# Kernel optimization log

Hardware: AMD Instinct MI355X
Metric: run time of the kernel (lower is better)

The kernel has to match this reference:

```python
import jax, jax.numpy as jnp
import numpy as np

D_MODEL, D_HIDDEN, N_EXPERTS, TOP_K = 1024, 2048, 8, 2


def setup_inputs() -> dict:
    key = jax.random.key(0)
    ks = jax.random.split(key, 8)
    s_in = 1.0 / np.sqrt(D_MODEL)
    s_hid = 1.0 / np.sqrt(D_HIDDEN)
    return {
        "x": jax.random.normal(ks[0], (1, 2048, D_MODEL), dtype=jnp.float32),
        # stacked expert weights, stored (in, out) so y = x @ W + b
        "W1": jax.random.normal(ks[1], (N_EXPERTS, D_MODEL, D_HIDDEN), dtype=jnp.float32) * s_in,
        "b1": jnp.zeros((N_EXPERTS, D_HIDDEN), dtype=jnp.float32),
        "W2": jax.random.normal(ks[2], (N_EXPERTS, D_MODEL, D_HIDDEN), dtype=jnp.float32) * s_in,
        "b2": jnp.zeros((N_EXPERTS, D_HIDDEN), dtype=jnp.float32),
        "Wo": jax.random.normal(ks[3], (N_EXPERTS, D_HIDDEN, D_MODEL), dtype=jnp.float32) * s_hid,
        "bo": jnp.zeros((N_EXPERTS, D_MODEL), dtype=jnp.float32),
        "Wr": jax.random.normal(ks[4], (D_MODEL, N_EXPERTS), dtype=jnp.float32) * s_in,
        "br": jnp.zeros((N_EXPERTS,), dtype=jnp.float32),
    }


def reference(x, W1, b1, W2, b2, Wo, bo, Wr, br):
    B, S, D = x.shape
    T = B * S
    xf = x.reshape(T, D)

    # router
    logits = xf @ Wr + br                      # [T, E]
    probs = jax.nn.softmax(logits, axis=-1)
    topk_probs, topk_idx = jax.lax.top_k(probs, TOP_K)  # [T, K]

    # combine weights: c[t, e] = sum_k topk_probs[t, k] * 1[topk_idx[t, k] == e]
    c = jnp.zeros((T, N_EXPERTS), dtype=xf.dtype)
    c = c.at[jnp.arange(T)[:, None], topk_idx].add(topk_probs)  # [T, E]

    # per-expert SwiGLU FFN applied densely, then masked-combined (same math
    # as the original gather/scatter loop since c[t,e]=0 for unrouted experts)
    h = jnp.einsum('td,edh->eth', xf, W1) + b1[:, None, :]   # [E, T, H]
    g = jnp.einsum('td,edh->eth', xf, W2) + b2[:, None, :]
    y = jnp.einsum('eth,ehd->etd', h * jax.nn.silu(g), Wo) + bo[:, None, :]
    out = jnp.einsum('etd,te->td', y, c).reshape(B, S, D)

    probs_mean = probs.mean(axis=0)
    lb_loss = (probs_mean * probs_mean).sum() * N_EXPERTS
    return out, lb_loss
```

## Files before the change

### kernel.cpp

```cpp
#include <hip/hip_runtime.h>
#include <hip/hip_bf16.h>

#define T_TOK 2048
#define DM 1024
#define DH 2048
#define NE 8

using bf16x8 = __attribute__((ext_vector_type(8))) short;
using f32x4  = __attribute__((ext_vector_type(4))) float;

__device__ __forceinline__ unsigned short f2bf(float f) {
  union { float f; unsigned u; } v; v.f = f;
  unsigned r = v.u + 0x7FFFu + ((v.u >> 16) & 1u);
  return (unsigned short)(r >> 16);
}
__device__ __forceinline__ unsigned pk2(float a, float b) {
  return (unsigned)f2bf(a) | ((unsigned)f2bf(b) << 16);
}

__global__ void k_init(int* __restrict__ cnt) {
  if (threadIdx.x < NE) cnt[threadIdx.x] = 0;
}

__global__ __launch_bounds__(64) void k_router(
    const float* __restrict__ x, const float* __restrict__ Wr, const float* __restrict__ br,
    int* __restrict__ cnt, int* __restrict__ idx, float* __restrict__ wgt,
    int* __restrict__ t2r, float* __restrict__ probs, unsigned short* __restrict__ xb)
{
  const int t = blockIdx.x, l = threadIdx.x;
  float xv[16];
#pragma unroll
  for (int i = 0; i < 16; ++i) xv[i] = x[t*DM + l + 64*i];
#pragma unroll
  for (int i = 0; i < 16; ++i) xb[t*DM + l + 64*i] = f2bf(xv[i]);

  float acc[8] = {0.f,0.f,0.f,0.f,0.f,0.f,0.f,0.f};
#pragma unroll
  for (int i = 0; i < 16; ++i) {
    const float4* wp = (const float4*)&Wr[(size_t)(l + 64*i)*NE];
    float4 wa = wp[0], wb = wp[1];
    acc[0] += xv[i]*wa.x; acc[1] += xv[i]*wa.y; acc[2] += xv[i]*wa.z; acc[3] += xv[i]*wa.w;
    acc[4] += xv[i]*wb.x; acc[5] += xv[i]*wb.y; acc[6] += xv[i]*wb.z; acc[7] += xv[i]*wb.w;
  }
#pragma unroll
  for (int e = 0; e < 8; ++e) {
#pragma unroll
    for (int off = 32; off; off >>= 1) acc[e] += __shfl_xor(acc[e], off, 64);
    acc[e] += br[e];
  }
  float mx = acc[0];
#pragma unroll
  for (int e = 1; e < 8; ++e) mx = fmaxf(mx, acc[e]);
  float p[8], s = 0.f;
#pragma unroll
  for (int e = 0; e < 8; ++e) { p[e] = expf(acc[e] - mx); s += p[e]; }
  float inv = 1.f / s;
#pragma unroll
  for (int e = 0; e < 8; ++e) p[e] *= inv;

  int e0 = 0; float p0 = p[0];
#pragma unroll
  for (int e = 1; e < 8; ++e) if (p[e] > p0) { p0 = p[e]; e0 = e; }
  int e1 = -1; float p1 = -1.f;
#pragma unroll
  for (int e = 0; e < 8; ++e) { if (e == e0) continue; if (p[e] > p1) { p1 = p[e]; e1 = e; } }

  if (l == 0) {
#pragma unroll
    for (int e = 0; e < 8; ++e) probs[t*NE + e] = p[e];
    int pos0 = atomicAdd(&cnt[e0], 1);
    idx[e0*T_TOK + pos0] = t; wgt[e0*T_TOK + pos0] = p0;
    t2r[t*2 + 0] = e0*T_TOK + pos0;
    int pos1 = atomicAdd(&cnt[e1], 1);
    idx[e1*T_TOK + pos1] = t; wgt[e1*T_TOK + pos1] = p1;
    t2r[t*2 + 1] = e1*T_TOK + pos1;
  }
}

__global__ __launch_bounds__(256) void k_finalize(
    const int* __restrict__ cnt, int* __restrict__ rb,
    const float* __restrict__ probs, float* __restrict__ out)
{
  __shared__ float red[8][256];
  const int tid = threadIdx.x;
  float s[8] = {0.f,0.f,0.f,0.f,0.f,0.f,0.f,0.f};
  for (int t = tid; t < T_TOK; t += 256) {
#pragma unroll
    for (int e = 0; e < 8; ++e) s[e] += probs[t*NE + e];
  }
#pragma unroll
  for (int e = 0; e < 8; ++e) red[e][tid] = s[e];
  __syncthreads();
  for (int w = 128; w > 0; w >>= 1) {
    if (tid < w) {
#pragma unroll
      for (int e = 0; e < 8; ++e) red[e][tid] += red[e][tid + w];
    }
    __syncthreads();
  }
  if (tid == 0) {
    float lb = 0.f;
#pragma unroll
    for (int e = 0; e < 8; ++e) {
      float mean = red[e][0] * (1.f / T_TOK);
      lb += mean * mean;
    }
    out[2097152] = lb * NE;
    int r = 0;
#pragma unroll
    for (int e = 0; e < 8; ++e) { rb[e] = r; r += cnt[e]; }
  }
}

#define TM1 128
#define TN1 64
#define BKK 64

__global__ __launch_bounds__(256) void k_ffn1(
    const unsigned short* __restrict__ xb,
    const float* __restrict__ W1, const float* __restrict__ b1,
    const float* __restrict__ W2, const float* __restrict__ b2,
    const int* __restrict__ cnt, const int* __restrict__ rbp,
    const int* __restrict__ idx, unsigned short* __restrict__ act)
{
  const int e = blockIdx.z, mt = blockIdx.y, nt = blockIdx.x;
  const int Me = cnt[e];
  const int m0 = mt * TM1;
  if (m0 >= Me) return;
  const int n0 = nt * TN1;

  __shared__ __align__(16) unsigned short As[TM1*BKK];
  __shared__ __align__(16) unsigned short Bh[TN1*BKK];
  __shared__ __align__(16) unsigned short Bg[TN1*BKK];
  __shared__ int toks[TM1];

  const int tid = threadIdx.x;
  if (tid < TM1) toks[tid] = idx[e*T_TOK + min(m0 + tid, Me - 1)];
  __syncthreads();

  const int lane = tid & 63;
  const int wave = tid >> 6;
  const int wm = wave >> 1, wn = wave & 1;
  const int row16 = lane & 15, kg = lane >> 4;

  f32x4 ah[4][2], ag[4][2];
#pragma unroll
  for (int i = 0; i < 4; ++i)
#pragma unroll
    for (int j = 0; j < 2; ++j) { ah[i][j] = 0.f; ag[i][j] = 0.f; }

  for (int k0 = 0; k0 < DM; k0 += BKK) {
#pragma unroll
    for (int it = 0; it < 4; ++it) {
      int task = tid + it*256;
      int r = task >> 3, sl = task & 7;
      uint4 v = *(const uint4*)&xb[(size_t)toks[r]*DM + k0 + sl*8];
      *(uint4*)&As[r*BKK + ((sl ^ (r & 7)) * 8)] = v;
    }
#pragma unroll
    for (int it = 0; it < 2; ++it) {
      int task = tid + it*256;
      int n = task & 63, kq = (task >> 6) & 7;
      size_t gb = ((size_t)e*DM + (size_t)(k0 + kq*8)) * DH + (n0 + n);
      {
        float f0=W1[gb], f1=W1[gb+DH], f2=W1[gb+2*DH], f3=W1[gb+3*DH];
        float f4=W1[gb+4*DH], f5=W1[gb+5*DH], f6=W1[gb+6*DH], f7=W1[gb+7*DH];
        uint4 v; v.x=pk2(f0,f1); v.y=pk2(f2,f3); v.z=pk2(f4,f5); v.w=pk2(f6,f7);
        *(uint4*)&Bh[n*BKK + ((kq ^ (n & 7)) * 8)] = v;
      }
      {
        float f0=W2[gb], f1=W2[gb+DH], f2=W2[gb+2*DH], f3=W2[gb+3*DH];
        float f4=W2[gb+4*DH], f5=W2[gb+5*DH], f6=W2[gb+6*DH], f7=W2[gb+7*DH];
        uint4 v; v.x=pk2(f0,f1); v.y=pk2(f2,f3); v.z=pk2(f4,f5); v.w=pk2(f6,f7);
        *(uint4*)&Bg[n*BKK + ((kq ^ (n & 7)) * 8)] = v;
      }
    }
    __syncthreads();
#pragma unroll
    for (int ks = 0; ks < 2; ++ks) {
      const int kslot = ks*4 + kg;
      bf16x8 a[4], vbh[2], vbg[2];
#pragma unroll
      for (int mi = 0; mi < 4; ++mi) {
        int m = wm*64 + mi*16 + row16;
        a[mi] = *(const bf16x8*)&As[m*BKK + ((kslot ^ (m & 7)) * 8)];
      }
#pragma unroll
      for (int ni = 0; ni < 2; ++ni) {
        int n = wn*32 + ni*16 + row16;
        int off = n*BKK + ((kslot ^ (n & 7)) * 8);
        vbh[ni] = *(const bf16x8*)&Bh[off];
        vbg[ni] = *(const bf16x8*)&Bg[off];
      }
#pragma unroll
      for (int mi = 0; mi < 4; ++mi)
#pragma unroll
        for (int ni = 0; ni < 2; ++ni) {
          ah[mi][ni] = __builtin_amdgcn_mfma_f32_16x16x32_bf16(a[mi], vbh[ni], ah[mi][ni], 0, 0, 0);
          ag[mi][ni] = __builtin_amdgcn_mfma_f32_16x16x32_bf16(a[mi], vbg[ni], ag[mi][ni], 0, 0, 0);
        }
    }
    __syncthreads();
  }

  const int rb = rbp[e];
#pragma unroll
  for (int mi = 0; mi < 4; ++mi) {
#pragma unroll
    for (int i = 0; i < 4; ++i) {
      int rloc = wm*64 + mi*16 + (lane >> 4)*4 + i;
      int m = m0 + rloc;
      if (m < Me) {
#pragma unroll
        for (int ni = 0; ni < 2; ++ni) {
          int col = n0 + wn*32 + ni*16 + row16;
          float h = ah[mi][ni][i] + b1[e*DH + col];
          float g = ag[mi][ni][i] + b2[e*DH + col];
          float sg = g / (1.f + __expf(-g));
          act[(size_t)(rb + m)*DH + col] = f2bf(h * sg);
        }
      }
    }
  }
}

__global__ __launch_bounds__(256) void k_ffn2(
    const unsigned short* __restrict__ act,
    const float* __restrict__ Wo, const float* __restrict__ bo,
    const int* __restrict__ cnt, const int* __restrict__ rbp,
    float* __restrict__ ys)
{
  const int e = blockIdx.z, mt = blockIdx.y, nt = blockIdx.x;
  const int Me = cnt[e];
  const int m0 = mt * TM1;
  if (m0 >= Me) return;
  const int n0 = nt * TN1;
  const int rb = rbp[e];

  __shared__ __align__(16) unsigned short As[TM1*BKK];
  __shared__ __align__(16) unsigned short Bs[TN1*BKK];

  const int tid = threadIdx.x;
  const int lane = tid & 63;
  const int wave = tid >> 6;
  const int wm = wave >> 1, wn = wave & 1;
  const int row16 = lane & 15, kg = lane >> 4;

  f32x4 acc[4][2];
#pragma unroll
  for (int i = 0; i < 4; ++i)
#pragma unroll
    for (int j = 0; j < 2; ++j) acc[i][j] = 0.f;

  for (int k0 = 0; k0 < DH; k0 += BKK) {
#pragma unroll
    for (int it = 0; it < 4; ++it) {
      int task = tid + it*256;
      int r = task >> 3, sl = task & 7;
      int grow = rb + min(m0 + r, Me - 1);
      uint4 v = *(const uint4*)&act[(size_t)grow*DH + k0 + sl*8];
      *(uint4*)&As[r*BKK + ((sl ^ (r & 7)) * 8)] = v;
    }
#pragma unroll
    for (int it = 0; it < 2; ++it) {
      int task = tid + it*256;
      int n = task & 63, kq = (task >> 6) & 7;
      size_t gb = ((size_t)e*DH + (size_t)(k0 + kq*8)) * DM + (n0 + n);
      float f0=Wo[gb], f1=Wo[gb+DM], f2=Wo[gb+2*DM], f3=Wo[gb+3*DM];
      float f4=Wo[gb+4*DM], f5=Wo[gb+5*DM], f6=Wo[gb+6*DM], f7=Wo[gb+7*DM];
      uint4 v; v.x=pk2(f0,f1); v.y=pk2(f2,f3); v.z=pk2(f4,f5); v.w=pk2(f6,f7);
      *(uint4*)&Bs[n*BKK + ((kq ^ (n & 7)) * 8)] = v;
    }
    __syncthreads();
#pragma unroll
    for (int ks = 0; ks < 2; ++ks) {
      const int kslot = ks*4 + kg;
      bf16x8 a[4], b[2];
#pragma unroll
      for (int mi = 0; mi < 4; ++mi) {
        int m = wm*64 + mi*16 + row16;
        a[mi] = *(const bf16x8*)&As[m*BKK + ((kslot ^ (m & 7)) * 8)];
      }
#pragma unroll
      for (int ni = 0; ni < 2; ++ni) {
        int n = wn*32 + ni*16 + row16;
        b[ni] = *(const bf16x8*)&Bs[n*BKK + ((kslot ^ (n & 7)) * 8)];
      }
#pragma unroll
      for (int mi = 0; mi < 4; ++mi)
#pragma unroll
        for (int ni = 0; ni < 2; ++ni)
          acc[mi][ni] = __builtin_amdgcn_mfma_f32_16x16x32_bf16(a[mi], b[ni], acc[mi][ni], 0, 0, 0);
    }
    __syncthreads();
  }

#pragma unroll
  for (int mi = 0; mi < 4; ++mi) {
#pragma unroll
    for (int i = 0; i < 4; ++i) {
      int rloc = wm*64 + mi*16 + (lane >> 4)*4 + i;
      int m = m0 + rloc;
      if (m < Me) {
#pragma unroll
        for (int ni = 0; ni < 2; ++ni) {
          int col = n0 + wn*32 + ni*16 + row16;
          ys[(size_t)(rb + m)*DM + col] = acc[mi][ni][i] + bo[e*DM + col];
        }
      }
    }
  }
}

__global__ __launch_bounds__(256) void k_combine(
    const float* __restrict__ ys, const int* __restrict__ t2r,
    const int* __restrict__ rbp, const float* __restrict__ wgt,
    float* __restrict__ out)
{
  const int t = blockIdx.x, tid = threadIdx.x;
  const int c0 = t2r[t*2 + 0], c1 = t2r[t*2 + 1];
  const float w0 = wgt[c0], w1 = wgt[c1];
  const int r0 = rbp[c0 >> 11] + (c0 & 2047);
  const int r1 = rbp[c1 >> 11] + (c1 & 2047);
  const float4* p0 = (const float4*)&ys[(size_t)r0*DM];
  const float4* p1 = (const float4*)&ys[(size_t)r1*DM];
  float4* po = (float4*)&out[(size_t)t*DM];
  float4 a = p0[tid], b = p1[tid];
  float4 r;
  r.x = w0*a.x + w1*b.x; r.y = w0*a.y + w1*b.y;
  r.z = w0*a.z + w1*b.z; r.w = w0*a.w + w1*b.w;
  po[tid] = r;
}

extern "C" void kernel_launch(void* const* d_in, const int* in_sizes, int n_in,
                              void* d_out, int out_size, void* d_ws, size_t ws_size,
                              hipStream_t stream)
{
  const float* x  = (const float*)d_in[0];
  const float* W1 = (const float*)d_in[1];
  const float* b1 = (const float*)d_in[2];
  const float* W2 = (const float*)d_in[3];
  const float* b2 = (const float*)d_in[4];
  const float* Wo = (const float*)d_in[5];
  const float* bo = (const float*)d_in[6];
  const float* Wr = (const float*)d_in[7];
  const float* br = (const float*)d_in[8];
  float* out = (float*)d_out;

  char* ws = (char*)d_ws;
  int*   cnt   = (int*)(ws + 0);
  int*   rb    = (int*)(ws + 256);
  int*   t2r   = (int*)(ws + 512);
  int*   idx   = (int*)(ws + 32*1024);
  float* wgt   = (float*)(ws + 96*1024);
  float* probs = (float*)(ws + 160*1024);
  unsigned short* xb  = (unsigned short*)(ws + 256*1024);
  unsigned short* act = (unsigned short*)(ws + 5ull*1024*1024);
  float* ysb = (float*)(ws + 21ull*1024*1024);

  k_init<<<1, 64, 0, stream>>>(cnt);
  k_router<<<T_TOK, 64, 0, stream>>>(x, Wr, br, cnt, idx, wgt, t2r, probs, xb);
  k_finalize<<<1, 256, 0, stream>>>(cnt, rb, probs, out);
  k_ffn1<<<dim3(DH/TN1, T_TOK/TM1, NE), 256, 0, stream>>>(xb, W1, b1, W2, b2, cnt, rb, idx, act);
  k_ffn2<<<dim3(DM/TN1, T_TOK/TM1, NE), 256, 0, stream>>>(act, Wo, bo, cnt, rb, ysb);
  k_combine<<<T_TOK, 256, 0, stream>>>(ysb, t2r, rb, wgt, out);
}
```

Measured before the change: 224.1 us.

## Pre-transpose expert weights to bf16 and stream GEMM tiles via global_load_lds

Adds a transpose-and-convert kernel that rewrites W1, W2 and Wo each call into bf16, K-contiguous copies held in workspace. New FFN GEMM kernels load A and B tiles straight into XOR-swizzled LDS with 16-byte global_load_lds, instead of loading fp32 weights and converting them inside the GEMM. The aim is to halve weight bytes per tile reload and drop in-loop conversion and register staging. The price is a full extra pass that reads the fp32 weights and writes the bf16 copies on every call. The new path runs only when the workspace holds at least 136 MB, otherwise the old kernels run.

```diff
diff --git a/kernel.cpp b/kernel.cpp
--- a/kernel.cpp
+++ b/kernel.cpp
@@ -17,6 +17,11 @@
 __device__ __forceinline__ unsigned pk2(float a, float b) {
   return (unsigned)f2bf(a) | ((unsigned)f2bf(b) << 16);
 }
+
+#define GLOAD16(gsrc, ldst)                                                        \
+  __builtin_amdgcn_global_load_lds(                                                \
+      (const __attribute__((address_space(1))) unsigned int*)(gsrc),               \
+      (__attribute__((address_space(3))) unsigned int*)(ldst), 16, 0, 0)
 
 __global__ void k_init(int* __restrict__ cnt) {
   if (threadIdx.x < NE) cnt[threadIdx.x] = 0;
@@ -112,9 +117,223 @@
   }
 }
 
+__global__ __launch_bounds__(256) void k_convT(
+    const float* __restrict__ in, unsigned short* __restrict__ outT, int R, int C)
+{
+  const int e = blockIdx.z;
+  const int r0 = blockIdx.y * 64, c0 = blockIdx.x * 64;
+  __shared__ float t[64][65];
+  const int tid = threadIdx.x;
+  const int lr = tid >> 4, lc = (tid & 15) * 4;
+#pragma unroll
+  for (int i = 0; i < 4; ++i) {
+    float4 v = *(const float4*)&in[((size_t)e*R + r0 + lr + i*16)*C + c0 + lc];
+    t[lr + i*16][lc+0] = v.x; t[lr + i*16][lc+1] = v.y;
+    t[lr + i*16][lc+2] = v.z; t[lr + i*16][lc+3] = v.w;
+  }
+  __syncthreads();
+  const int oc = tid >> 3;
+  const int od = (tid & 7) * 8;
+#pragma unroll
+  for (int i = 0; i < 2; ++i) {
+    int c = oc + i*32;
+    uint4 v;
+    v.x = pk2(t[od+0][c], t[od+1][c]);
+    v.y = pk2(t[od+2][c], t[od+3][c]);
+    v.z = pk2(t[od+4][c], t[od+5][c]);
+    v.w = pk2(t[od+6][c], t[od+7][c]);
+    *(uint4*)&outT[((size_t)e*C + c0 + c)*R + r0 + od] = v;
+  }
+}
+
 #define TM1 128
 #define TN1 64
 #define BKK 64
+
+
+__global__ __launch_bounds__(256) void k_ffn1b(
+    const unsigned short* __restrict__ xb,
+    const unsigned short* __restrict__ W1T, const float* __restrict__ b1,
+    const unsigned short* __restrict__ W2T, const float* __restrict__ b2,
+    const int* __restrict__ cnt, const int* __restrict__ rbp,
+    const int* __restrict__ idx, unsigned short* __restrict__ act)
+{
+  const int e = blockIdx.z, mt = blockIdx.y, nt = blockIdx.x;
+  const int Me = cnt[e];
+  const int m0 = mt * TM1;
+  if (m0 >= Me) return;
+  const int n0 = nt * TN1;
+
+  __shared__ __align__(16) unsigned short As[TM1*BKK];
+  __shared__ __align__(16) unsigned short Bh[TN1*BKK];
+  __shared__ __align__(16) unsigned short Bg[TN1*BKK];
+  __shared__ int toks[TM1];
+
+  const int tid = threadIdx.x;
+  if (tid < TM1) toks[tid] = idx[e*T_TOK + min(m0 + tid, Me - 1)];
+  __syncthreads();
+
+  const int lane = tid & 63;
+  const int wave = tid >> 6;
+  const int wm = wave >> 1, wn = wave & 1;
+  const int row16 = lane & 15, kg = lane >> 4;
+  const int sl = lane & 7;
+  const int lr = lane >> 3;
+
+  f32x4 ah[4][2], ag[4][2];
+#pragma unroll
+  for (int i = 0; i < 4; ++i)
+#pragma unroll
+    for (int j = 0; j < 2; ++j) { ah[i][j] = 0.f; ag[i][j] = 0.f; }
+
+  for (int k0 = 0; k0 < DM; k0 += BKK) {
+#pragma unroll
+    for (int i = 0; i < 4; ++i) {
+      int r = (wave*4 + i)*8 + lr;
+      const unsigned short* src = &xb[(size_t)toks[r]*DM + k0 + ((sl ^ (r & 7)) * 8)];
+      GLOAD16(src, &As[(wave*4 + i)*512]);
+    }
+#pragma unroll
+    for (int j = 0; j < 2; ++j) {
+      int r = (wave*2 + j)*8 + lr;
+      size_t gb = ((size_t)e*DH + n0 + r)*DM + k0 + ((sl ^ (r & 7)) * 8);
+      GLOAD16(&W1T[gb], &Bh[(wave*2 + j)*512]);
+      GLOAD16(&W2T[gb], &Bg[(wave*2 + j)*512]);
+    }
+    __syncthreads();
+#pragma unroll
+    for (int ks = 0; ks < 2; ++ks) {
+      const int kslot = ks*4 + kg;
+      bf16x8 a[4], vbh[2], vbg[2];
+#pragma unroll
+      for (int mi = 0; mi < 4; ++mi) {
+        int m = wm*64 + mi*16 + row16;
+        a[mi] = *(const bf16x8*)&As[m*BKK + ((kslot ^ (m & 7)) * 8)];
+      }
+#pragma unroll
+      for (int ni = 0; ni < 2; ++ni) {
+        int n = wn*32 + ni*16 + row16;
+        int off = n*BKK + ((kslot ^ (n & 7)) * 8);
+        vbh[ni] = *(const bf16x8*)&Bh[off];
+        vbg[ni] = *(const bf16x8*)&Bg[off];
+      }
+#pragma unroll
+      for (int mi = 0; mi < 4; ++mi)
+#pragma unroll
+        for (int ni = 0; ni < 2; ++ni) {
+          ah[mi][ni] = __builtin_amdgcn_mfma_f32_16x16x32_bf16(a[mi], vbh[ni], ah[mi][ni], 0, 0, 0);
+          ag[mi][ni] = __builtin_amdgcn_mfma_f32_16x16x32_bf16(a[mi], vbg[ni], ag[mi][ni], 0, 0, 0);
+        }
+    }
+    __syncthreads();
+  }
+
+  const int rb = rbp[e];
+#pragma unroll
+  for (int mi = 0; mi < 4; ++mi) {
+#pragma unroll
+    for (int i = 0; i < 4; ++i) {
+      int rloc = wm*64 + mi*16 + (lane >> 4)*4 + i;
+      int m = m0 + rloc;
+      if (m < Me) {
+#pragma unroll
+        for (int ni = 0; ni < 2; ++ni) {
+          int col = n0 + wn*32 + ni*16 + row16;
+          float h = ah[mi][ni][i] + b1[e*DH + col];
+          float g = ag[mi][ni][i] + b2[e*DH + col];
+          float sg = g / (1.f + __expf(-g));
+          act[(size_t)(rb + m)*DH + col] = f2bf(h * sg);
+        }
+      }
+    }
+  }
+}
+
+__global__ __launch_bounds__(256) void k_ffn2b(
+    const unsigned short* __restrict__ act,
+    const unsigned short* __restrict__ WoT, const float* __restrict__ bo,
+    const int* __restrict__ cnt, const int* __restrict__ rbp,
+    float* __restrict__ ys)
+{
+  const int e = blockIdx.z, mt = blockIdx.y, nt = blockIdx.x;
+  const int Me = cnt[e];
+  const int m0 = mt * TM1;
+  if (m0 >= Me) return;
+  const int n0 = nt * TN1;
+  const int rb = rbp[e];
+
+  __shared__ __align__(16) unsigned short As[TM1*BKK];
+  __shared__ __align__(16) unsigned short Bs[TN1*BKK];
+
+  const int tid = threadIdx.x;
+  const int lane = tid & 63;
+  const int wave = tid >> 6;
+  const int wm = wave >> 1, wn = wave & 1;
+  const int row16 = lane & 15, kg = lane >> 4;
+  const int sl = lane & 7;
+  const int lr = lane >> 3;
+
+  f32x4 acc[4][2];
+#pragma unroll
+  for (int i = 0; i < 4; ++i)
+#pragma unroll
+    for (int j = 0; j < 2; ++j) acc[i][j] = 0.f;
+
+  for (int k0 = 0; k0 < DH; k0 += BKK) {
+#pragma unroll
+    for (int i = 0; i < 4; ++i) {
+      int r = (wave*4 + i)*8 + lr;
+      int grow = rb + min(m0 + r, Me - 1);
+      const unsigned short* src = &act[(size_t)grow*DH + k0 + ((sl ^ (r & 7)) * 8)];
+      GLOAD16(src, &As[(wave*4 + i)*512]);
+    }
+#pragma unroll
+    for (int j = 0; j < 2; ++j) {
+      int r = (wave*2 + j)*8 + lr;
+      size_t gb = ((size_t)e*DM + n0 + r)*DH + k0 + ((sl ^ (r & 7)) * 8);
+      GLOAD16(&WoT[gb], &Bs[(wave*2 + j)*512]);
+    }
+    __syncthreads();
+#pragma unroll
+    for (int ks = 0; ks < 2; ++ks) {
+      const int kslot = ks*4 + kg;
+      bf16x8 a[4], b[2];
+#pragma unroll
+      for (int mi = 0; mi < 4; ++mi) {
+        int m = wm*64 + mi*16 + row16;
+        a[mi] = *(const bf16x8*)&As[m*BKK + ((kslot ^ (m & 7)) * 8)];
+      }
+#pragma unroll
+      for (int ni = 0; ni < 2; ++ni) {
+        int n = wn*32 + ni*16 + row16;
+        b[ni] = *(const bf16x8*)&Bs[n*BKK + ((kslot ^ (n & 7)) * 8)];
+      }
+#pragma unroll
+      for (int mi = 0; mi < 4; ++mi)
+#pragma unroll
+        for (int ni = 0; ni < 2; ++ni)
+          acc[mi][ni] = __builtin_amdgcn_mfma_f32_16x16x32_bf16(a[mi], b[ni], acc[mi][ni], 0, 0, 0);
+    }
+    __syncthreads();
+  }
+
+#pragma unroll
+  for (int mi = 0; mi < 4; ++mi) {
+#pragma unroll
+    for (int i = 0; i < 4; ++i) {
+      int rloc = wm*64 + mi*16 + (lane >> 4)*4 + i;
+      int m = m0 + rloc;
+      if (m < Me) {
+#pragma unroll
+        for (int ni = 0; ni < 2; ++ni) {
+          int col = n0 + wn*32 + ni*16 + row16;
+          ys[(size_t)(rb + m)*DM + col] = acc[mi][ni][i] + bo[e*DM + col];
+        }
+      }
+    }
+  }
+}
+
 
 __global__ __launch_bounds__(256) void k_ffn1(
     const unsigned short* __restrict__ xb,
@@ -357,11 +576,24 @@
   unsigned short* xb  = (unsigned short*)(ws + 256*1024);
   unsigned short* act = (unsigned short*)(ws + 5ull*1024*1024);
   float* ysb = (float*)(ws + 21ull*1024*1024);
+  unsigned short* W1T = (unsigned short*)(ws + 40ull*1024*1024);
+  unsigned short* W2T = (unsigned short*)(ws + 72ull*1024*1024);
+  unsigned short* WoT = (unsigned short*)(ws + 104ull*1024*1024);
+  const bool fast = ws_size >= 136ull*1024*1024;
 
   k_init<<<1, 64, 0, stream>>>(cnt);
   k_router<<<T_TOK, 64, 0, stream>>>(x, Wr, br, cnt, idx, wgt, t2r, probs, xb);
   k_finalize<<<1, 256, 0, stream>>>(cnt, rb, probs, out);
-  k_ffn1<<<dim3(DH/TN1, T_TOK/TM1, NE), 256, 0, stream>>>(xb, W1, b1, W2, b2, cnt, rb, idx, act);
-  k_ffn2<<<dim3(DM/TN1, T_TOK/TM1, NE), 256, 0, stream>>>(act, Wo, bo, cnt, rb, ysb);
+
+  if (fast) {
+    k_convT<<<dim3(DH/64, DM/64, NE), 256, 0, stream>>>(W1, W1T, DM, DH);
+    k_convT<<<dim3(DH/64, DM/64, NE), 256, 0, stream>>>(W2, W2T, DM, DH);
+    k_convT<<<dim3(DM/64, DH/64, NE), 256, 0, stream>>>(Wo, WoT, DH, DM);
+    k_ffn1b<<<dim3(DH/TN1, T_TOK/TM1, NE), 256, 0, stream>>>(xb, W1T, b1, W2T, b2, cnt, rb, idx, act);
+    k_ffn2b<<<dim3(DM/TN1, T_TOK/TM1, NE), 256, 0, stream>>>(act, WoT, bo, cnt, rb, ysb);
+  } else {
+    k_ffn1<<<dim3(DH/TN1, T_TOK/TM1, NE), 256, 0, stream>>>(xb, W1, b1, W2, b2, cnt, rb, idx, act);
+    k_ffn2<<<dim3(DM/TN1, T_TOK/TM1, NE), 256, 0, stream>>>(act, Wo, bo, cnt, rb, ysb);
+  }
   k_combine<<<T_TOK, 256, 0, stream>>>(ysb, t2r, rb, wgt, out);
 }
```

New measurement: 223.1 us. No clear change (-0.4%).

## Pre-transpose weights to bf16 and double-buffer GEMM tiles via direct global-to-LDS loads

Applied to the files above, without the earlier changes.

Adds a conversion kernel that transposes and converts W1, W2 and Wo to bf16 once per call. The expert GEMMs can then stream contiguous bf16 rows straight into LDS with global_load_lds into double-buffered tiles, which overlaps the next tile's load with the current MFMA work. The goal is to remove the strided fp32 weight gathers and per-element conversions from the GEMM inner loops. In exchange, every call reads all weights in fp32 and writes them back in bf16 before the GEMMs start. The router is also repacked to four tokens per 256-thread block.

```diff
diff --git a/kernel.cpp b/kernel.cpp
--- a/kernel.cpp
+++ b/kernel.cpp
@@ -18,16 +18,22 @@
   return (unsigned)f2bf(a) | ((unsigned)f2bf(b) << 16);
 }
 
+#define GLOAD16(gsrc, ldst)                                                        \
+  __builtin_amdgcn_global_load_lds(                                                \
+      (const __attribute__((address_space(1))) unsigned int*)(gsrc),               \
+      (__attribute__((address_space(3))) unsigned int*)(ldst), 16, 0, 0)
+
 __global__ void k_init(int* __restrict__ cnt) {
   if (threadIdx.x < NE) cnt[threadIdx.x] = 0;
 }
 
-__global__ __launch_bounds__(64) void k_router(
+__global__ __launch_bounds__(256) void k_router(
     const float* __restrict__ x, const float* __restrict__ Wr, const float* __restrict__ br,
     int* __restrict__ cnt, int* __restrict__ idx, float* __restrict__ wgt,
     int* __restrict__ t2r, float* __restrict__ probs, unsigned short* __restrict__ xb)
 {
-  const int t = blockIdx.x, l = threadIdx.x;
+  const int wave = threadIdx.x >> 6, l = threadIdx.x & 63;
+  const int t = blockIdx.x * 4 + wave;
   float xv[16];
 #pragma unroll
   for (int i = 0; i < 16; ++i) xv[i] = x[t*DM + l + 64*i];
@@ -112,14 +118,54 @@
   }
 }
 
+__global__ __launch_bounds__(256) void k_convAll(
+    const float* __restrict__ W1, const float* __restrict__ W2, const float* __restrict__ Wo,
+    unsigned short* __restrict__ W1T, unsigned short* __restrict__ W2T,
+    unsigned short* __restrict__ WoT)
+{
+  int b = blockIdx.x;
+  const float* in; unsigned short* outT; int R, C;
+  if (b < 4096)      { in = W1; outT = W1T; R = DM; C = DH; }
+  else if (b < 8192) { in = W2; outT = W2T; R = DM; C = DH; b -= 4096; }
+  else               { in = Wo; outT = WoT; R = DH; C = DM; b -= 8192; }
+  const int nC = C / 64;
+  const int tilesPerE = (R / 64) * nC;
+  const int e  = b / tilesPerE;
+  const int tb = b % tilesPerE;
+  const int r0 = (tb / nC) * 64, c0 = (tb % nC) * 64;
+
+  __shared__ float t[64][65];
+  const int tid = threadIdx.x;
+  const int lr = tid >> 4, lc = (tid & 15) * 4;
+#pragma unroll
+  for (int i = 0; i < 4; ++i) {
+    float4 v = *(const float4*)&in[((size_t)e*R + r0 + lr + i*16)*C + c0 + lc];
+    t[lr + i*16][lc+0] = v.x; t[lr + i*16][lc+1] = v.y;
+    t[lr + i*16][lc+2] = v.z; t[lr + i*16][lc+3] = v.w;
+  }
+  __syncthreads();
+  const int oc = tid >> 3;
+  const int od = (tid & 7) * 8;
+#pragma unroll
+  for (int i = 0; i < 2; ++i) {
+    int c = oc + i*32;
+    uint4 v;
+    v.x = pk2(t[od+0][c], t[od+1][c]);
+    v.y = pk2(t[od+2][c], t[od+3][c]);
+    v.z = pk2(t[od+4][c], t[od+5][c]);
+    v.w = pk2(t[od+6][c], t[od+7][c]);
+    *(uint4*)&outT[((size_t)e*C + c0 + c)*R + r0 + od] = v;
+  }
+}
+
 #define TM1 128
 #define TN1 64
 #define BKK 64
 
-__global__ __launch_bounds__(256) void k_ffn1(
+__global__ __launch_bounds__(256) void k_ffn1b(
     const unsigned short* __restrict__ xb,
-    const float* __restrict__ W1, const float* __restrict__ b1,
-    const float* __restrict__ W2, const float* __restrict__ b2,
+    const unsigned short* __restrict__ W1T, const float* __restrict__ b1,
+    const unsigned short* __restrict__ W2T, const float* __restrict__ b2,
     const int* __restrict__ cnt, const int* __restrict__ rbp,
     const int* __restrict__ idx, unsigned short* __restrict__ act)
 {
@@ -129,9 +175,9 @@
   if (m0 >= Me) return;
   const int n0 = nt * TN1;
 
-  __shared__ __align__(16) unsigned short As[TM1*BKK];
-  __shared__ __align__(16) unsigned short Bh[TN1*BKK];
-  __shared__ __align__(16) unsigned short Bg[TN1*BKK];
+  __shared__ __align__(16) unsigned short As[2][TM1*BKK];
+  __shared__ __align__(16) unsigned short Bh[2][TN1*BKK];
+  __shared__ __align__(16) unsigned short Bg[2][TN1*BKK];
   __shared__ int toks[TM1];
 
   const int tid = threadIdx.x;
@@ -142,6 +188,34 @@
   const int wave = tid >> 6;
   const int wm = wave >> 1, wn = wave & 1;
   const int row16 = lane & 15, kg = lane >> 4;
+  const int sl = lane & 7;
+  const int lr = lane >> 3;
+
+  const unsigned short* asrc[4];
+#pragma unroll
+  for (int i = 0; i < 4; ++i) {
+    int r = (wave*4 + i)*8 + lr;
+    asrc[i] = &xb[(size_t)toks[r]*DM + ((sl ^ (r & 7)) * 8)];
+  }
+  const unsigned short *bsrc1[2], *bsrc2[2];
+#pragma unroll
+  for (int j = 0; j < 2; ++j) {
+    int r = (wave*2 + j)*8 + lr;
+    size_t gb = ((size_t)e*DH + n0 + r)*DM + ((sl ^ (r & 7)) * 8);
+    bsrc1[j] = &W1T[gb]; bsrc2[j] = &W2T[gb];
+  }
+
+#define STAGE1(buf, k0)                                                   \
+  do {                                                                    \
+    _Pragma("unroll")                                                     \
+    for (int i = 0; i < 4; ++i)                                           \
+      GLOAD16(asrc[i] + (k0), &As[buf][(wave*4 + i)*512]);                \
+    _Pragma("unroll")                                                     \
+    for (int j = 0; j < 2; ++j) {                                         \
+      GLOAD16(bsrc1[j] + (k0), &Bh[buf][(wave*2 + j)*512]);               \
+      GLOAD16(bsrc2[j] + (k0), &Bg[buf][(wave*2 + j)*512]);               \
+    }                                                                     \
+  } while (0)
 
   f32x4 ah[4][2], ag[4][2];
 #pragma unroll
@@ -149,33 +223,12 @@
 #pragma unroll
     for (int j = 0; j < 2; ++j) { ah[i][j] = 0.f; ag[i][j] = 0.f; }
 
-  for (int k0 = 0; k0 < DM; k0 += BKK) {
-#pragma unroll
-    for (int it = 0; it < 4; ++it) {
-      int task = tid + it*256;
-      int r = task >> 3, sl = task & 7;
-      uint4 v = *(const uint4*)&xb[(size_t)toks[r]*DM + k0 + sl*8];
-      *(uint4*)&As[r*BKK + ((sl ^ (r & 7)) * 8)] = v;
-    }
-#pragma unroll
-    for (int it = 0; it < 2; ++it) {
-      int task = tid + it*256;
-      int n = task & 63, kq = (task >> 6) & 7;
-      size_t gb = ((size_t)e*DM + (size_t)(k0 + kq*8)) * DH + (n0 + n);
-      {
-        float f0=W1[gb], f1=W1[gb+DH], f2=W1[gb+2*DH], f3=W1[gb+3*DH];
-        float f4=W1[gb+4*DH], f5=W1[gb+5*DH], f6=W1[gb+6*DH], f7=W1[gb+7*DH];
-        uint4 v; v.x=pk2(f0,f1); v.y=pk2(f2,f3); v.z=pk2(f4,f5); v.w=pk2(f6,f7);
-        *(uint4*)&Bh[n*BKK + ((kq ^ (n & 7)) * 8)] = v;
-      }
-      {
-        float f0=W2[gb], f1=W2[gb+DH], f2=W2[gb+2*DH], f3=W2[gb+3*DH];
-        float f4=W2[gb+4*DH], f5=W2[gb+5*DH], f6=W2[gb+6*DH], f7=W2[gb+7*DH];
-        uint4 v; v.x=pk2(f0,f1); v.y=pk2(f2,f3); v.z=pk2(f4,f5); v.w=pk2(f6,f7);
-        *(uint4*)&Bg[n*BKK + ((kq ^ (n & 7)) * 8)] = v;
-      }
-    }
-    __syncthreads();
+  STAGE1(0, 0);
+  __syncthreads();
+
+  for (int kt = 0; kt < DM/BKK; ++kt) {
+    const int cur = kt & 1;
+    if (kt + 1 < DM/BKK) STAGE1(cur ^ 1, (kt + 1) * BKK);
 #pragma unroll
     for (int ks = 0; ks < 2; ++ks) {
       const int kslot = ks*4 + kg;
@@ -183,14 +236,14 @@
 #pragma unroll
       for (int mi = 0; mi < 4; ++mi) {
         int m = wm*64 + mi*16 + row16;
-        a[mi] = *(const bf16x8*)&As[m*BKK + ((kslot ^ (m & 7)) * 8)];
+        a[mi] = *(const bf16x8*)&As[cur][m*BKK + ((kslot ^ (m & 7)) * 8)];
       }
 #pragma unroll
       for (int ni = 0; ni < 2; ++ni) {
         int n = wn*32 + ni*16 + row16;
         int off = n*BKK + ((kslot ^ (n & 7)) * 8);
-        vbh[ni] = *(const bf16x8*)&Bh[off];
-        vbg[ni] = *(const bf16x8*)&Bg[off];
+        vbh[ni] = *(const bf16x8*)&Bh[cur][off];
+        vbg[ni] = *(const bf16x8*)&Bg[cur][off];
       }
 #pragma unroll
       for (int mi = 0; mi < 4; ++mi)
@@ -222,11 +275,12 @@
       }
     }
   }
-}
-
-__global__ __launch_bounds__(256) void k_ffn2(
+#undef STAGE1
+}
+
+__global__ __launch_bounds__(256) void k_ffn2b(
     const unsigned short* __restrict__ act,
-    const float* __restrict__ Wo, const float* __restrict__ bo,
+    const unsigned short* __restrict__ WoT, const float* __restrict__ bo,
     const int* __restrict__ cnt, const int* __restrict__ rbp,
     float* __restrict__ ys)
 {
@@ -237,14 +291,40 @@
   const int n0 = nt * TN1;
   const int rb = rbp[e];
 
-  __shared__ __align__(16) unsigned short As[TM1*BKK];
-  __shared__ __align__(16) unsigned short Bs[TN1*BKK];
+  __shared__ __align__(16) unsigned short As[2][TM1*BKK];
+  __shared__ __align__(16) unsigned short Bs[2][TN1*BKK];
 
   const int tid = threadIdx.x;
   const int lane = tid & 63;
   const int wave = tid >> 6;
   const int wm = wave >> 1, wn = wave & 1;
   const int row16 = lane & 15, kg = lane >> 4;
+  const int sl = lane & 7;
+  const int lr = lane >> 3;
+
+  const unsigned short* asrc[4];
+#pragma unroll
+  for (int i = 0; i < 4; ++i) {
+    int r = (wave*4 + i)*8 + lr;
+    int grow = rb + min(m0 + r, Me - 1);
+    asrc[i] = &act[(size_t)grow*DH + ((sl ^ (r & 7)) * 8)];
+  }
+  const unsigned short* bsrc[2];
+#pragma unroll
+  for (int j = 0; j < 2; ++j) {
+    int r = (wave*2 + j)*8 + lr;
+    bsrc[j] = &WoT[((size_t)e*DM + n0 + r)*DH + ((sl ^ (r & 7)) * 8)];
+  }
+
+#define STAGE2(buf, k0)                                                   \
+  do {                                                                    \
+    _Pragma("unroll")                                                     \
+    for (int i = 0; i < 4; ++i)                                           \
+      GLOAD16(asrc[i] + (k0), &As[buf][(wave*4 + i)*512]);                \
+    _Pragma("unroll")                                                     \
+    for (int j = 0; j < 2; ++j)                                           \
+      GLOAD16(bsrc[j] + (k0), &Bs[buf][(wave*2 + j)*512]);                \
+  } while (0)
 
   f32x4 acc[4][2];
 #pragma unroll
@@ -252,26 +332,12 @@
 #pragma unroll
     for (int j = 0; j < 2; ++j) acc[i][j] = 0.f;
 
-  for (int k0 = 0; k0 < DH; k0 += BKK) {
-#pragma unroll
-    for (int it = 0; it < 4; ++it) {
-      int task = tid + it*256;
-      int r = task >> 3, sl = task & 7;
-      int grow = rb + min(m0 + r, Me - 1);
-      uint4 v = *(const uint4*)&act[(size_t)grow*DH + k0 + sl*8];
-      *(uint4*)&As[r*BKK + ((sl ^ (r & 7)) * 8)] = v;
-    }
-#pragma unroll
-    for (int it = 0; it < 2; ++it) {
-      int task = tid + it*256;
-      int n = task & 63, kq = (task >> 6) & 7;
-      size_t gb = ((size_t)e*DH + (size_t)(k0 + kq*8)) * DM + (n0 + n);
-      float f0=Wo[gb], f1=Wo[gb+DM], f2=Wo[gb+2*DM], f3=Wo[gb+3*DM];
-      float f4=Wo[gb+4*DM], f5=Wo[gb+5*DM], f6=Wo[gb+6*DM], f7=Wo[gb+7*DM];
-      uint4 v; v.x=pk2(f0,f1); v.y=pk2(f2,f3); v.z=pk2(f4,f5); v.w=pk2(f6,f7);
-      *(uint4*)&Bs[n*BKK + ((kq ^ (n & 7)) * 8)] = v;
-    }
-    __syncthreads();
+  STAGE2(0, 0);
+  __syncthreads();
+
+  for (int kt = 0; kt < DH/BKK; ++kt) {
+    const int cur = kt & 1;
+    if (kt + 1 < DH/BKK) STAGE2(cur ^ 1, (kt + 1) * BKK);
 #pragma unroll
     for (int ks = 0; ks < 2; ++ks) {
       const int kslot = ks*4 + kg;
@@ -279,12 +345,12 @@
 #pragma unroll
       for (int mi = 0; mi < 4; ++mi) {
         int m = wm*64 + mi*16 + row16;
-        a[mi] = *(const bf16x8*)&As[m*BKK + ((kslot ^ (m & 7)) * 8)];
+        a[mi] = *(const bf16x8*)&As[cur][m*BKK + ((kslot ^ (m & 7)) * 8)];
       }
 #pragma unroll
       for (int ni = 0; ni < 2; ++ni) {
         int n = wn*32 + ni*16 + row16;
-        b[ni] = *(const bf16x8*)&Bs[n*BKK + ((kslot ^ (n & 7)) * 8)];
+        b[ni] = *(const bf16x8*)&Bs[cur][n*BKK + ((kslot ^ (n & 7)) * 8)];
       }
 #pragma unroll
       for (int mi = 0; mi < 4; ++mi)
@@ -310,6 +376,7 @@
       }
     }
   }
+#undef STAGE2
 }
 
 __global__ __launch_bounds__(256) void k_combine(
@@ -357,11 +424,15 @@
   unsigned short* xb  = (unsigned short*)(ws + 256*1024);
   unsigned short* act = (unsigned short*)(ws + 5ull*1024*1024);
   float* ysb = (float*)(ws + 21ull*1024*1024);
+  unsigned short* W1T = (unsigned short*)(ws + 40ull*1024*1024);
+  unsigned short* W2T = (unsigned short*)(ws + 72ull*1024*1024);
+  unsigned short* WoT = (unsigned short*)(ws + 104ull*1024*1024);
 
   k_init<<<1, 64, 0, stream>>>(cnt);
-  k_router<<<T_TOK, 64, 0, stream>>>(x, Wr, br, cnt, idx, wgt, t2r, probs, xb);
+  k_router<<<T_TOK/4, 256, 0, stream>>>(x, Wr, br, cnt, idx, wgt, t2r, probs, xb);
   k_finalize<<<1, 256, 0, stream>>>(cnt, rb, probs, out);
-  k_ffn1<<<dim3(DH/TN1, T_TOK/TM1, NE), 256, 0, stream>>>(xb, W1, b1, W2, b2, cnt, rb, idx, act);
-  k_ffn2<<<dim3(DM/TN1, T_TOK/TM1, NE), 256, 0, stream>>>(act, Wo, bo, cnt, rb, ysb);
+  k_convAll<<<12288, 256, 0, stream>>>(W1, W2, Wo, W1T, W2T, WoT);
+  k_ffn1b<<<dim3(DH/TN1, T_TOK/TM1, NE), 256, 0, stream>>>(xb, W1T, b1, W2T, b2, cnt, rb, idx, act);
+  k_ffn2b<<<dim3(DM/TN1, T_TOK/TM1, NE), 256, 0, stream>>>(act, WoT, bo, cnt, rb, ysb);
   k_combine<<<T_TOK, 256, 0, stream>>>(ysb, t2r, rb, wgt, out);
 }
```

Result: no change. 225.9 us (+0.8%).
